# Performance work log

Hardware: AMD Instinct MI355X
Metric: run time of the kernel (lower is better)

Reference implementation:

```python
import jax, jax.numpy as jnp
import numpy as np

# config (matches init_kwargs)
B, H, N, D = 2, 8, 2048, 64
ALPHA = 1.0        # < 2 -> power-law kernel branch
D_INT = 4.0        # d_intrinsic
BW = 1.0           # bandwidth
A = 0.5            # dual-sided degree-normalization exponent
R = 1.0            # sphere_radius
MASK_VAL = 10000.0
EPS = 1e-7


def setup_inputs() -> dict:
    key = jax.random.key(0)
    k1, k2, k3, k4 = jax.random.split(key, 4)
    Q = jax.random.normal(k1, (B, H, N, D), dtype=jnp.float32)
    K = jax.random.normal(k2, (B, H, N, D), dtype=jnp.float32)
    V = jax.random.normal(k3, (B, H, N, D), dtype=jnp.float32)
    mask = jax.random.randint(k4, (B, N), 0, 2).astype(jnp.int32)
    return {"Q": Q, "K": K, "V": V, "mask": mask}


def reference(Q, K, V, mask) -> jnp.ndarray:
    # geodesic distance on the sphere: acos(clamp(QK^T)) * radius  [B,H,N,N]
    qk = jnp.einsum('bhnd,bhmd->bhnm', Q, K)
    g_dist = jnp.arccos(jnp.clip(qk, -1.0 + EPS, 1.0 - EPS)) * R
    # key-side padding mask: [B,N] -> [B,1,1,N]
    g_dist = jnp.where(mask[:, None, None, :] == 0, MASK_VAL, g_dist)
    # power-law kernel (alpha < 2 branch)
    attn_score = (1.0 + g_dist / jnp.sqrt(BW)) ** (-D_INT - ALPHA)
    # dual-sided degree normalization (a != 0 branch)
    n_r = jnp.sum(attn_score, axis=-1)   # row degrees [B,H,N]
    n_c = jnp.sum(attn_score, axis=-2)   # col degrees [B,H,N]
    k_tilde = (n_r ** (-A))[..., :, None] * attn_score * (n_c ** (-A))[..., None, :]
    # F.normalize(p=1, dim=3)
    attn = k_tilde / jnp.maximum(jnp.sum(jnp.abs(k_tilde), axis=-1, keepdims=True), 1e-12)
    # dropout p=0.0 -> identity
    return jnp.einsum('bhnm,bhmd->bhnd', attn, V)
```

## Files before the change

kernel.cpp:

```cpp
#include <hip/hip_runtime.h>
#include <hip/hip_bf16.h>
#include <math.h>

#define B_ 2
#define H_ 8
#define N_ 2048
#define D_ 64
#define BH_ 16
#define NT_ (N_/64)
#define LS 72
#define LSW (LS/2)

typedef __attribute__((ext_vector_type(8))) short short8;
typedef __attribute__((ext_vector_type(4))) float float4v;

__device__ __forceinline__ unsigned packbf2(float a, float b){
  __hip_bfloat162 h = __float22bfloat162_rn(make_float2(a, b));
  return *(unsigned*)&h;
}
__device__ __forceinline__ void split2(float a, float b, unsigned& hi, unsigned& lo){
  hi = packbf2(a, b);
  float ha = __uint_as_float(hi << 16);
  float hb = __uint_as_float(hi & 0xFFFF0000u);
  lo = packbf2(a - ha, b - hb);
}
__device__ __forceinline__ void load_split8(const float* p, short8& hi8, short8& lo8){
  float4v v0 = *(const float4v*)p;
  float4v v1 = *(const float4v*)(p + 4);
  unsigned h0,h1,h2,h3,l0,l1,l2,l3;
  split2(v0.x, v0.y, h0, l0);
  split2(v0.z, v0.w, h1, l1);
  split2(v1.x, v1.y, h2, l2);
  split2(v1.z, v1.w, h3, l3);
  unsigned ph[4] = {h0,h1,h2,h3};
  unsigned pl[4] = {l0,l1,l2,l3};
  hi8 = *(short8*)ph;
  lo8 = *(short8*)pl;
}

__device__ __forceinline__ float score_fn(float qk, float masked){
  float ax = fminf(fabsf(qk), 1.0f - 1e-7f);
  float t  = __builtin_amdgcn_sqrtf(1.0f - ax);
  float p  = __builtin_fmaf(__builtin_fmaf(__builtin_fmaf(-0.0187293f, ax, 0.0742610f),
                                           ax, -0.2121144f), ax, 1.5707288f);
  float t2 = t * p;
  float g  = (qk >= 0.0f) ? t2 : (3.14159265358979f - t2);
  g = (masked != 0.0f) ? 10000.0f : g;
  float w1 = 1.0f + g;
  float w2 = w1*w1;
  float w4 = w2*w2;
  float w5 = w4*w1;
  return __builtin_amdgcn_rcpf(w5);
}

template<bool STORE>
__global__ __launch_bounds__(256) void k1_score(
    const float* __restrict__ Q, const float* __restrict__ K,
    const int* __restrict__ mask, float* __restrict__ ncw,
    unsigned short* __restrict__ S)
{
  __shared__ float msk[64];
  __shared__ float red[64*4];

  const int kt = blockIdx.x, bh = blockIdx.y, rz = blockIdx.z;
  const int nz = gridDim.z;
  const int tid = threadIdx.x;
  const int wv = tid>>6, lane = tid&63, quad = lane>>4, l15 = lane&15;

  const float* Qg = Q + (size_t)bh*N_*D_;
  const float* Kg = K + (size_t)bh*N_*D_;

  short8 khi[4][2], klo[4][2];
  #pragma unroll
  for (int s=0;s<4;++s){
    const float* kp = Kg + (size_t)(kt*64 + s*16 + l15)*D_ + quad*8;
    load_split8(kp,      khi[s][0], klo[s][0]);
    load_split8(kp + 32, khi[s][1], klo[s][1]);
  }
  if (tid < 64)
    msk[tid] = (mask[(bh>>3)*N_ + kt*64 + tid] == 0) ? 1.f : 0.f;
  __syncthreads();

  float cs[4][4];
  #pragma unroll
  for (int s=0;s<4;++s)
    #pragma unroll
    for (int i=0;i<4;++i) cs[s][i] = 0.f;

  const int iters = NT_/nz;
  for (int rti=0; rti<iters; ++rti){
    const int rt = rz*iters + rti;
    const float* qp = Qg + (size_t)(rt*64 + wv*16 + l15)*D_ + quad*8;
    short8 bhi[2], blo[2];
    load_split8(qp,      bhi[0], blo[0]);
    load_split8(qp + 32, bhi[1], blo[1]);

    const size_t nrow = (size_t)(bh*NT_ + kt)*N_ + (size_t)rt*64 + wv*16 + l15;
    #pragma unroll
    for (int s=0;s<4;++s){
      float4v c = {0.f,0.f,0.f,0.f};
      #pragma unroll
      for (int cc=0; cc<2; ++cc){
        c = __builtin_amdgcn_mfma_f32_16x16x32_bf16(khi[s][cc], bhi[cc], c, 0,0,0);
        c = __builtin_amdgcn_mfma_f32_16x16x32_bf16(khi[s][cc], blo[cc], c, 0,0,0);
        c = __builtin_amdgcn_mfma_f32_16x16x32_bf16(klo[s][cc], bhi[cc], c, 0,0,0);
      }
      int kl = s*16 + quad*4;
      float sc0 = score_fn(c[0], msk[kl+0]);
      float sc1 = score_fn(c[1], msk[kl+1]);
      float sc2 = score_fn(c[2], msk[kl+2]);
      float sc3 = score_fn(c[3], msk[kl+3]);
      cs[s][0]+=sc0; cs[s][1]+=sc1; cs[s][2]+=sc2; cs[s][3]+=sc3;
      if (STORE){
        uint2 pk;
        pk.x = packbf2(sc0, sc1);
        pk.y = packbf2(sc2, sc3);
        *(uint2*)&S[nrow*64 + kl] = pk;
      }
    }
  }

  #pragma unroll
  for (int s=0;s<4;++s)
    #pragma unroll
    for (int i=0;i<4;++i){
      float v2 = cs[s][i];
      v2 += __shfl_xor(v2, 1);
      v2 += __shfl_xor(v2, 2);
      v2 += __shfl_xor(v2, 4);
      v2 += __shfl_xor(v2, 8);
      cs[s][i] = v2;
    }
  if (l15 == 0){
    #pragma unroll
    for (int s=0;s<4;++s)
      #pragma unroll
      for (int i=0;i<4;++i)
        red[(s*16 + quad*4 + i)*4 + wv] = cs[s][i];
  }
  __syncthreads();
  if (tid < 64){
    float t = red[tid*4+0] + red[tid*4+1] + red[tid*4+2] + red[tid*4+3];
    if (STORE) atomicAdd(&ncw[bh*N_ + kt*64 + tid], t);
    else       ncw[bh*N_ + kt*64 + tid] = 1.0f / sqrtf(t);
  }
}

__global__ __launch_bounds__(256) void k2_pack(
    const float* __restrict__ V, const float* __restrict__ nc,
    unsigned short* __restrict__ Vw)
{
  __shared__ float T[64*65];
  __shared__ float wrow[64];
  const int mt = blockIdx.x, bh = blockIdx.y;
  const int tid = threadIdx.x;
  const float* Vg = V + (size_t)bh*N_*D_;
  const float* ncg = nc + (size_t)bh*N_;
  unsigned short* Fb = Vw + ((size_t)(bh*NT_ + mt)*10)*512;

  {
    int m = tid >> 2;
    int d0 = (tid & 3) * 16;
    int gm = mt*64 + m;
    float wm = 1.0f / sqrtf(fmaxf(ncg[gm], 1e-30f));
    if (d0 == 0) wrow[m] = wm;
    #pragma unroll
    for (int j=0;j<4;++j){
      float4v v = *(const float4v*)(Vg + (size_t)gm*D_ + d0 + j*4);
      T[(d0+j*4+0)*65 + m] = v.x*wm;
      T[(d0+j*4+1)*65 + m] = v.y*wm;
      T[(d0+j*4+2)*65 + m] = v.z*wm;
      T[(d0+j*4+3)*65 + m] = v.w*wm;
    }
  }
  __syncthreads();

  for (int idx = tid; idx < 640; idx += 256){
    int f = idx >> 6, lane = idx & 63;
    int quad = lane >> 4, l15 = lane & 15;
    int s2 = f >> 1, cc = f & 1;
    int m0 = cc*32 + quad*8;
    unsigned pk[4];
    if (s2 < 4){
      int d = s2*16 + l15;
      #pragma unroll
      for (int j=0;j<4;++j)
        pk[j] = packbf2(T[d*65 + m0 + 2*j], T[d*65 + m0 + 2*j + 1]);
    } else if (l15 == 0){
      #pragma unroll
      for (int j=0;j<4;++j)
        pk[j] = packbf2(wrow[m0 + 2*j], wrow[m0 + 2*j + 1]);
    } else {
      pk[0]=pk[1]=pk[2]=pk[3]=0u;
    }
    *(short8*)(Fb + ((size_t)f*64 + lane)*8) = *(short8*)pk;
  }
}

__global__ __launch_bounds__(1024) void k3_stream(
    const unsigned short* __restrict__ S, const unsigned short* __restrict__ Vw,
    float* __restrict__ out)
{
  __shared__ float Red[4*3*16*68];

  const int rt = blockIdx.x, bh = blockIdx.y;
  const int tid = threadIdx.x;
  const int wvid = tid >> 6;
  const int sr = wvid & 3;
  const int kc = wvid >> 2;
  const int lane = tid & 63, quad = lane>>4, l15 = lane&15;

  float4v acc[4];
  #pragma unroll
  for (int i=0;i<4;++i) acc[i] = (float4v){0.f,0.f,0.f,0.f};
  float4v c5 = {0.f,0.f,0.f,0.f};

  const size_t srow = (size_t)rt*64 + sr*16 + l15;

  short8 npf0, npf1;
  {
    const size_t sbase = ((size_t)(bh*NT_ + kc*8)*N_ + srow)*64;
    npf0 = *(const short8*)&S[sbase +  0 + quad*8];
    npf1 = *(const short8*)&S[sbase + 32 + quad*8];
  }

  for (int ki=0; ki<8; ++ki){
    const int kt = kc*8 + ki;
    short8 pf0 = npf0, pf1 = npf1;
    {
      const int ktn = kc*8 + (ki < 7 ? ki+1 : 7);
      const size_t sb = ((size_t)(bh*NT_ + ktn)*N_ + srow)*64;
      npf0 = *(const short8*)&S[sb +  0 + quad*8];
      npf1 = *(const short8*)&S[sb + 32 + quad*8];
    }
    const unsigned short* F = Vw + ((size_t)(bh*NT_ + kt)*10)*512 + (size_t)lane*8;
    #pragma unroll
    for (int s2=0;s2<4;++s2){
      const short8 a0 = *(const short8*)(F + (size_t)(s2*2+0)*512);
      const short8 a1 = *(const short8*)(F + (size_t)(s2*2+1)*512);
      acc[s2] = __builtin_amdgcn_mfma_f32_16x16x32_bf16(a0, pf0, acc[s2], 0,0,0);
      acc[s2] = __builtin_amdgcn_mfma_f32_16x16x32_bf16(a1, pf1, acc[s2], 0,0,0);
    }
    {
      const short8 a0 = *(const short8*)(F + (size_t)8*512);
      const short8 a1 = *(const short8*)(F + (size_t)9*512);
      c5 = __builtin_amdgcn_mfma_f32_16x16x32_bf16(a0, pf0, c5, 0,0,0);
      c5 = __builtin_amdgcn_mfma_f32_16x16x32_bf16(a1, pf1, c5, 0,0,0);
    }
  }

  if (kc > 0){
    float* Rr = Red + ((size_t)((sr*3 + (kc-1))*16) + l15)*68;
    #pragma unroll
    for (int s2=0;s2<4;++s2)
      #pragma unroll
      for (int i=0;i<4;++i)
        Rr[s2*16 + quad*4 + i] = acc[s2][i];
    if (quad == 0) Rr[64] = c5[0];
  }
  __syncthreads();
  if (kc == 0){
    #pragma unroll
    for (int p=0; p<3; ++p){
      const float* Rr = Red + ((size_t)((sr*3 + p)*16) + l15)*68;
      #pragma unroll
      for (int s2=0;s2<4;++s2)
        #pragma unroll
        for (int i=0;i<4;++i)
          acc[s2][i] += Rr[s2*16 + quad*4 + i];
    }
    float rs = __shfl(c5[0], l15);
    #pragma unroll
    for (int p=0; p<3; ++p)
      rs += Red[((size_t)((sr*3 + p)*16) + l15)*68 + 64];
    float inv = 1.0f / fmaxf(rs, 1e-12f);

    float* Og = out + (size_t)bh*N_*D_ + (size_t)(rt*64 + sr*16 + l15)*D_;
    #pragma unroll
    for (int s2=0;s2<4;++s2)
      #pragma unroll
      for (int i=0;i<4;++i)
        Og[s2*16 + quad*4 + i] = acc[s2][i] * inv;
  }
}

__global__ __launch_bounds__(256) void spop_pass2(
    const float* __restrict__ Q, const float* __restrict__ K,
    const float* __restrict__ V, const int* __restrict__ mask,
    const float* __restrict__ w, float* __restrict__ out)
{
  __shared__ unsigned short Khi[64*LS], Klo[64*LS];
  __shared__ unsigned short Vt[64*LS];
  __shared__ unsigned short Ps[64*LS];
  __shared__ float msk[64], wms[64];

  const int rt = blockIdx.x, bh = blockIdx.y, b = bh>>3;
  const int tid = threadIdx.x;
  const int wv = tid>>6, lane = tid&63, quad = lane>>4, l15 = lane&15;

  const float* Qg = Q + (size_t)bh*N_*D_;
  const float* Kg = K + (size_t)bh*N_*D_;
  const float* Vg = V + (size_t)bh*N_*D_;

  short8 qhi[2], qlo[2];
  {
    const float* qp = Qg + (size_t)(rt*64 + wv*16 + l15)*D_ + quad*8;
    load_split8(qp,      qhi[0], qlo[0]);
    load_split8(qp + 32, qhi[1], qlo[1]);
  }

  float4v acc[4];
  #pragma unroll
  for (int i=0;i<4;++i) acc[i] = (float4v){0.f,0.f,0.f,0.f};
  float rs = 0.f;

  for (int kt=0; kt<NT_; ++kt){
    __syncthreads();
    #pragma unroll
    for (int it=0; it<4; ++it){
      int idx = tid + it*256;
      int r = idx>>4, d4 = (idx&15)<<2;
      const float4v v = *(const float4v*)(Kg + (size_t)(kt*64 + r)*D_ + d4);
      unsigned h0,l0,h1,l1;
      split2(v.x, v.y, h0, l0);
      split2(v.z, v.w, h1, l1);
      unsigned* KhiW = (unsigned*)Khi; unsigned* KloW = (unsigned*)Klo;
      int base = r*LSW + (d4>>1);
      KhiW[base] = h0; KhiW[base+1] = h1;
      KloW[base] = l0; KloW[base+1] = l1;
    }
    #pragma unroll
    for (int it=0; it<2; ++it){
      int u = tid + it*256;
      int kp = u & 31;
      int d4 = (u>>5)<<2;
      const float* vp = Vg + (size_t)(kt*64 + kp*2)*D_ + d4;
      float4v a0 = *(const float4v*)vp;
      float4v a1 = *(const float4v*)(vp + D_);
      unsigned* VtW = (unsigned*)Vt;
      VtW[(d4+0)*LSW + kp] = packbf2(a0.x, a1.x);
      VtW[(d4+1)*LSW + kp] = packbf2(a0.y, a1.y);
      VtW[(d4+2)*LSW + kp] = packbf2(a0.z, a1.z);
      VtW[(d4+3)*LSW + kp] = packbf2(a0.w, a1.w);
    }
    if (tid < 64){
      int gk = kt*64 + tid;
      msk[tid] = (mask[b*N_ + gk] == 0) ? 1.f : 0.f;
      wms[tid] = w[bh*N_ + gk];
    }
    __syncthreads();

    #pragma unroll
    for (int s=0;s<4;++s){
      float4v c = {0.f,0.f,0.f,0.f};
      #pragma unroll
      for (int cc=0; cc<2; ++cc){
        const short8 ahi = *(const short8*)&Khi[(s*16+l15)*LS + cc*32 + quad*8];
        const short8 alo = *(const short8*)&Klo[(s*16+l15)*LS + cc*32 + quad*8];
        c = __builtin_amdgcn_mfma_f32_16x16x32_bf16(ahi, qhi[cc], c, 0,0,0);
        c = __builtin_amdgcn_mfma_f32_16x16x32_bf16(ahi, qlo[cc], c, 0,0,0);
        c = __builtin_amdgcn_mfma_f32_16x16x32_bf16(alo, qhi[cc], c, 0,0,0);
      }
      int kl = s*16 + quad*4;
      float sc0 = score_fn(c[0], msk[kl+0]) * wms[kl+0];
      float sc1 = score_fn(c[1], msk[kl+1]) * wms[kl+1];
      float sc2 = score_fn(c[2], msk[kl+2]) * wms[kl+2];
      float sc3 = score_fn(c[3], msk[kl+3]) * wms[kl+3];
      rs += (sc0 + sc1) + (sc2 + sc3);
      unsigned* PsW = (unsigned*)Ps;
      int pb = (wv*16 + l15)*LSW + (kl>>1);
      PsW[pb]   = packbf2(sc0, sc1);
      PsW[pb+1] = packbf2(sc2, sc3);
    }

    short8 pf[2];
    pf[0] = *(const short8*)&Ps[(wv*16+l15)*LS +  0 + quad*8];
    pf[1] = *(const short8*)&Ps[(wv*16+l15)*LS + 32 + quad*8];
    #pragma unroll
    for (int s2=0;s2<4;++s2){
      #pragma unroll
      for (int cc=0; cc<2; ++cc){
        const short8 av = *(const short8*)&Vt[(s2*16+l15)*LS + cc*32 + quad*8];
        acc[s2] = __builtin_amdgcn_mfma_f32_16x16x32_bf16(av, pf[cc], acc[s2], 0,0,0);
      }
    }
  }

  rs += __shfl_xor(rs, 16);
  rs += __shfl_xor(rs, 32);
  float inv = 1.0f / fmaxf(rs, 1e-12f);

  float* Og = out + (size_t)bh*N_*D_ + (size_t)(rt*64 + wv*16 + l15)*D_;
  #pragma unroll
  for (int s2=0;s2<4;++s2)
    #pragma unroll
    for (int i=0;i<4;++i)
      Og[s2*16 + quad*4 + i] = acc[s2][i] * inv;
}

extern "C" void kernel_launch(void* const* d_in, const int* in_sizes, int n_in,
                              void* d_out, int out_size, void* d_ws, size_t ws_size,
                              hipStream_t stream) {
  (void)in_sizes; (void)n_in; (void)out_size;
  const float* Q   = (const float*)d_in[0];
  const float* K   = (const float*)d_in[1];
  const float* V   = (const float*)d_in[2];
  const int*  mask = (const int*)d_in[3];
  float* out = (float*)d_out;

  const size_t nc_bytes = (size_t)BH_*N_*sizeof(float);
  const size_t vw_off   = 131072;
  const size_t vw_bytes = (size_t)BH_*NT_*10*512*2;
  const size_t s_off    = vw_off + vw_bytes;
  const size_t S_bytes  = (size_t)2*BH_*N_*N_;
  const size_t need     = s_off + S_bytes;

  if (ws_size >= need){
    float* nc = (float*)d_ws;
    unsigned short* Vw = (unsigned short*)((char*)d_ws + vw_off);
    unsigned short* S  = (unsigned short*)((char*)d_ws + s_off);
    hipMemsetAsync(nc, 0, nc_bytes, stream);
    k1_score<true><<<dim3(NT_, BH_, 4), 256, 0, stream>>>(Q, K, mask, nc, S);
    k2_pack<<<dim3(NT_, BH_), 256, 0, stream>>>(V, nc, Vw);
    k3_stream<<<dim3(NT_, BH_), 1024, 0, stream>>>(S, Vw, out);
  } else {
    float* w = (float*)d_ws;
    k1_score<false><<<dim3(NT_, BH_, 1), 256, 0, stream>>>(Q, K, mask, w, nullptr);
    spop_pass2<<<dim3(NT_, BH_), 256, 0, stream>>>(Q, K, V, mask, w, out);
  }
}
```

Measured before the change: 195.5 us.

## Reuse V fragments across two row tiles per wave and reduce via LDS atomics

Each wave in the streaming PV kernel now handles two 16-row sub-tiles that share the same V fragment loads, and covers 4 key tiles instead of 8. This halves the V-fragment global loads per MFMA. The cross-wave split-K reduction now uses shared-memory atomic adds into one zeroed 64x67 accumulator instead of staging partials for a single wave to sum. The final normalize-and-store is spread over all threads with vectorized writes. In exchange it adds LDS atomic contention, an extra barrier for zero-initialisation, and higher register pressure per wave.

```diff
diff --git a/kernel.cpp b/kernel.cpp
--- a/kernel.cpp
+++ b/kernel.cpp
@@ -201,86 +201,96 @@
     const unsigned short* __restrict__ S, const unsigned short* __restrict__ Vw,
     float* __restrict__ out)
 {
-  __shared__ float Red[4*3*16*68];
+  __shared__ float Racc[64*67];
 
   const int rt = blockIdx.x, bh = blockIdx.y;
   const int tid = threadIdx.x;
   const int wvid = tid >> 6;
-  const int sr = wvid & 3;
-  const int kc = wvid >> 2;
+  const int sr2 = wvid & 1;
+  const int kc  = wvid >> 1;
   const int lane = tid & 63, quad = lane>>4, l15 = lane&15;
 
-  float4v acc[4];
-  #pragma unroll
-  for (int i=0;i<4;++i) acc[i] = (float4v){0.f,0.f,0.f,0.f};
-  float4v c5 = {0.f,0.f,0.f,0.f};
-
-  const size_t srow = (size_t)rt*64 + sr*16 + l15;
-
-  short8 npf0, npf1;
+  for (int z = tid; z < 64*67; z += 1024) Racc[z] = 0.f;
+
+  float4v accA[4], accB[4];
+  #pragma unroll
+  for (int i=0;i<4;++i){ accA[i] = (float4v){0.f,0.f,0.f,0.f}; accB[i] = (float4v){0.f,0.f,0.f,0.f}; }
+  float4v c5A = {0.f,0.f,0.f,0.f}, c5B = {0.f,0.f,0.f,0.f};
+
+  const size_t srowA = (size_t)rt*64 + sr2*32 + l15;
+  const size_t srowB = srowA + 16;
+
+  short8 nA0, nA1, nB0, nB1;
   {
-    const size_t sbase = ((size_t)(bh*NT_ + kc*8)*N_ + srow)*64;
-    npf0 = *(const short8*)&S[sbase +  0 + quad*8];
-    npf1 = *(const short8*)&S[sbase + 32 + quad*8];
-  }
-
-  for (int ki=0; ki<8; ++ki){
-    const int kt = kc*8 + ki;
-    short8 pf0 = npf0, pf1 = npf1;
+    const size_t ba = ((size_t)(bh*NT_ + kc*4)*N_ + srowA)*64;
+    const size_t bb = ((size_t)(bh*NT_ + kc*4)*N_ + srowB)*64;
+    nA0 = *(const short8*)&S[ba +  0 + quad*8];
+    nA1 = *(const short8*)&S[ba + 32 + quad*8];
+    nB0 = *(const short8*)&S[bb +  0 + quad*8];
+    nB1 = *(const short8*)&S[bb + 32 + quad*8];
+  }
+
+  __syncthreads();
+
+  for (int ki=0; ki<4; ++ki){
+    const int kt = kc*4 + ki;
+    short8 pA0 = nA0, pA1 = nA1, pB0 = nB0, pB1 = nB1;
     {
-      const int ktn = kc*8 + (ki < 7 ? ki+1 : 7);
-      const size_t sb = ((size_t)(bh*NT_ + ktn)*N_ + srow)*64;
-      npf0 = *(const short8*)&S[sb +  0 + quad*8];
-      npf1 = *(const short8*)&S[sb + 32 + quad*8];
+      const int ktn = kc*4 + (ki < 3 ? ki+1 : 3);
+      const size_t ba = ((size_t)(bh*NT_ + ktn)*N_ + srowA)*64;
+      const size_t bb = ((size_t)(bh*NT_ + ktn)*N_ + srowB)*64;
+      nA0 = *(const short8*)&S[ba +  0 + quad*8];
+      nA1 = *(const short8*)&S[ba + 32 + quad*8];
+      nB0 = *(const short8*)&S[bb +  0 + quad*8];
+      nB1 = *(const short8*)&S[bb + 32 + quad*8];
     }
     const unsigned short* F = Vw + ((size_t)(bh*NT_ + kt)*10)*512 + (size_t)lane*8;
     #pragma unroll
     for (int s2=0;s2<4;++s2){
       const short8 a0 = *(const short8*)(F + (size_t)(s2*2+0)*512);
       const short8 a1 = *(const short8*)(F + (size_t)(s2*2+1)*512);
-      acc[s2] = __builtin_amdgcn_mfma_f32_16x16x32_bf16(a0, pf0, acc[s2], 0,0,0);
-      acc[s2] = __builtin_amdgcn_mfma_f32_16x16x32_bf16(a1, pf1, acc[s2], 0,0,0);
+      accA[s2] = __builtin_amdgcn_mfma_f32_16x16x32_bf16(a0, pA0, accA[s2], 0,0,0);
+      accA[s2] = __builtin_amdgcn_mfma_f32_16x16x32_bf16(a1, pA1, accA[s2], 0,0,0);
+      accB[s2] = __builtin_amdgcn_mfma_f32_16x16x32_bf16(a0, pB0, accB[s2], 0,0,0);
+      accB[s2] = __builtin_amdgcn_mfma_f32_16x16x32_bf16(a1, pB1, accB[s2], 0,0,0);
     }
     {
-      const short8 a0 = *(const short8*)(F + (size_t)8*512);
-      const short8 a1 = *(const short8*)(F + (size_t)9*512);
-      c5 = __builtin_amdgcn_mfma_f32_16x16x32_bf16(a0, pf0, c5, 0,0,0);
-      c5 = __builtin_amdgcn_mfma_f32_16x16x32_bf16(a1, pf1, c5, 0,0,0);
-    }
-  }
-
-  if (kc > 0){
-    float* Rr = Red + ((size_t)((sr*3 + (kc-1))*16) + l15)*68;
+      const short8 a8 = *(const short8*)(F + (size_t)8*512);
+      const short8 a9 = *(const short8*)(F + (size_t)9*512);
+      c5A = __builtin_amdgcn_mfma_f32_16x16x32_bf16(a8, pA0, c5A, 0,0,0);
+      c5A = __builtin_amdgcn_mfma_f32_16x16x32_bf16(a9, pA1, c5A, 0,0,0);
+      c5B = __builtin_amdgcn_mfma_f32_16x16x32_bf16(a8, pB0, c5B, 0,0,0);
+      c5B = __builtin_amdgcn_mfma_f32_16x16x32_bf16(a9, pB1, c5B, 0,0,0);
+    }
+  }
+
+  {
+    const int rowA = sr2*32 + l15;
+    const int rowB = rowA + 16;
     #pragma unroll
     for (int s2=0;s2<4;++s2)
       #pragma unroll
-      for (int i=0;i<4;++i)
-        Rr[s2*16 + quad*4 + i] = acc[s2][i];
-    if (quad == 0) Rr[64] = c5[0];
+      for (int i=0;i<4;++i){
+        atomicAdd(&Racc[rowA*67 + s2*16 + quad*4 + i], accA[s2][i]);
+        atomicAdd(&Racc[rowB*67 + s2*16 + quad*4 + i], accB[s2][i]);
+      }
+    if (quad == 0){
+      atomicAdd(&Racc[rowA*67 + 64], c5A[0]);
+      atomicAdd(&Racc[rowB*67 + 64], c5B[0]);
+    }
   }
   __syncthreads();
-  if (kc == 0){
-    #pragma unroll
-    for (int p=0; p<3; ++p){
-      const float* Rr = Red + ((size_t)((sr*3 + p)*16) + l15)*68;
-      #pragma unroll
-      for (int s2=0;s2<4;++s2)
-        #pragma unroll
-        for (int i=0;i<4;++i)
-          acc[s2][i] += Rr[s2*16 + quad*4 + i];
-    }
-    float rs = __shfl(c5[0], l15);
-    #pragma unroll
-    for (int p=0; p<3; ++p)
-      rs += Red[((size_t)((sr*3 + p)*16) + l15)*68 + 64];
-    float inv = 1.0f / fmaxf(rs, 1e-12f);
-
-    float* Og = out + (size_t)bh*N_*D_ + (size_t)(rt*64 + sr*16 + l15)*D_;
-    #pragma unroll
-    for (int s2=0;s2<4;++s2)
-      #pragma unroll
-      for (int i=0;i<4;++i)
-        Og[s2*16 + quad*4 + i] = acc[s2][i] * inv;
+
+  {
+    const int row = tid >> 4;
+    const int c4  = (tid & 15) * 4;
+    const float inv = 1.0f / fmaxf(Racc[row*67 + 64], 1e-12f);
+    float4v o;
+    o.x = Racc[row*67 + c4 + 0] * inv;
+    o.y = Racc[row*67 + c4 + 1] * inv;
+    o.z = Racc[row*67 + c4 + 2] * inv;
+    o.w = Racc[row*67 + c4 + 3] * inv;
+    *(float4v*)(out + (size_t)bh*N_*D_ + (size_t)(rt*64 + row)*D_ + c4) = o;
   }
 }
 
```

Result: slower. 263.5 us (+34.8%).
